# Optimization experiments

Hardware: AMD Instinct MI355X
Metric: run time of the kernel (lower is better)

Reference implementation:

```python
import jax, jax.numpy as jnp
import numpy as np

B, C, H, W = 16, 256, 56, 56
HEADS, DHEAD = 8, 32
INNER = HEADS * DHEAD  # == C
BLOCK, HALO = 7, 3
WIN = BLOCK + 2 * HALO      # 13
REL = WIN                   # rel_size = block + 2*halo
HIDDEN = 4 * C
EPS = 1e-6
LS_INIT = 1e-6


def layernorm2d(x, w, b):
    # channels-first LayerNorm over C, x: (B,C,H,W)
    u = jnp.mean(x, axis=1, keepdims=True)
    s = jnp.mean((x - u) ** 2, axis=1, keepdims=True)
    xn = (x - u) * jax.lax.rsqrt(s + EPS)
    return w[None, :, None, None] * xn + b[None, :, None, None]


def rel_to_abs(x):
    # x: (b, l, 2r-1) -> (b, l, r)
    b, l, m = x.shape
    r = (m + 1) // 2
    x = jnp.pad(x, ((0, 0), (0, 0), (0, 1))).reshape(b, l * (m + 1))
    x = jnp.pad(x, ((0, 0), (0, m - l))).reshape(b, l + 1, m)
    return x[:, :l, -r:]


def relative_logits_1d(q, rel_k):
    # q: (b, h, w, d); rel_k: (2r-1, d) -> (b, h, r, w, r)
    b, h, w, _ = q.shape
    r = (rel_k.shape[0] + 1) // 2
    logits = jnp.einsum('bxyd,rd->bxyr', q, rel_k)
    logits = rel_to_abs(logits.reshape(b * h, w, -1)).reshape(b, h, w, r)
    return jnp.broadcast_to(logits[:, :, None], (b, h, r, w, r))


def rel_pos_bias(q, rel_h, rel_w):
    b = q.shape[0]
    r = (rel_w.shape[0] + 1) // 2
    q2 = q.reshape(b, BLOCK, BLOCK, DHEAD)
    lw = relative_logits_1d(q2, rel_w)                        # (b, x, i, y, j)
    lw = lw.transpose(0, 1, 3, 2, 4).reshape(b, BLOCK * BLOCK, r * r)
    lh = relative_logits_1d(q2.transpose(0, 2, 1, 3), rel_h)  # (b, y, i, x, j)
    lh = lh.transpose(0, 3, 1, 4, 2).reshape(b, BLOCK * BLOCK, r * r)
    return lw + lh


def halo_attention(x, wq, wkv, wo, bo, rel_h, rel_w):
    Bq, _, Hh, Ww = x.shape
    nh, nw = Hh // BLOCK, Ww // BLOCK
    nb = nh * nw
    # queries: non-overlapping blocks -> (B*nb, BLOCK^2, C)
    q_inp = x.reshape(Bq, C, nh, BLOCK, nw, BLOCK).transpose(0, 2, 4, 3, 5, 1)
    q_inp = q_inp.reshape(Bq * nb, BLOCK * BLOCK, C)
    # keys/values: overlapping haloed windows (like F.unfold with padding=HALO)
    xp = jnp.pad(x, ((0, 0), (0, 0), (HALO, HALO), (HALO, HALO)))
    rows = (jnp.arange(nh) * BLOCK)[:, None] + jnp.arange(WIN)
    cols = (jnp.arange(nw) * BLOCK)[:, None] + jnp.arange(WIN)
    kv = xp[:, :, rows][:, :, :, :, cols]
    kv = kv.transpose(0, 2, 4, 3, 5, 1).reshape(Bq * nb, WIN * WIN, C)
    q = q_inp @ wq.T
    k, v = jnp.split(kv @ wkv.T, 2, axis=-1)

    def split_heads(t):
        b2, n2, _ = t.shape
        return t.reshape(b2, n2, HEADS, DHEAD).transpose(0, 2, 1, 3).reshape(b2 * HEADS, n2, DHEAD)

    q, k, v = map(split_heads, (q, k, v))
    q = q * (DHEAD ** -0.5)
    sim = jnp.einsum('bid,bjd->bij', q, k) + rel_pos_bias(q, rel_h, rel_w)
    # mask out-of-bounds (zero-padded) halo positions
    onep = jnp.pad(jnp.ones((Hh, Ww), sim.dtype), ((HALO, HALO), (HALO, HALO)))
    m = (onep[rows][:, :, cols].transpose(0, 2, 1, 3).reshape(nb, WIN * WIN)) > 0
    sim = sim.reshape(Bq, nb, HEADS, BLOCK * BLOCK, WIN * WIN)
    sim = jnp.where(m[None, :, None, None, :], sim, -jnp.finfo(sim.dtype).max)
    sim = sim.reshape(Bq * nb * HEADS, BLOCK * BLOCK, WIN * WIN)
    attn = jax.nn.softmax(sim, axis=-1)
    out = jnp.einsum('bij,bjd->bid', attn, v)
    out = out.reshape(Bq * nb, HEADS, BLOCK * BLOCK, DHEAD).transpose(0, 2, 1, 3)
    out = out.reshape(Bq * nb, BLOCK * BLOCK, INNER) @ wo.T + bo
    out = out.reshape(Bq, nh, nw, BLOCK, BLOCK, C).transpose(0, 5, 1, 3, 2, 4)
    return out.reshape(Bq, C, Hh, Ww)


def _forward(x, ln1_w, ln1_b, ln2_w, ln2_b, wq, wkv, wo, bo, rel_h, rel_w,
             gamma1, gamma2, fc1_w, fc1_b, fc2_w, fc2_b):
    y = halo_attention(layernorm2d(x, ln1_w, ln1_b), wq, wkv, wo, bo, rel_h, rel_w)
    x = x + gamma1 * y  # drop_path = 0 -> identity
    z = layernorm2d(x, ln2_w, ln2_b).transpose(0, 2, 3, 1)  # NHWC
    z = jax.nn.gelu(z @ fc1_w.T + fc1_b, approximate=False)
    z = z @ fc2_w.T + fc2_b
    z = gamma2 * z
    return x + z.transpose(0, 3, 1, 2)


def setup_inputs() -> dict:
    key = jax.random.key(0)
    ks = jax.random.split(key, 8)
    n = lambda k, sh: jax.random.normal(k, sh, jnp.float32) * 0.02
    scale = DHEAD ** -0.5
    return dict(
        x=jax.random.normal(ks[0], (B, C, H, W), jnp.float32),
        ln1_w=jnp.ones((C,), jnp.float32), ln1_b=jnp.zeros((C,), jnp.float32),
        ln2_w=jnp.ones((C,), jnp.float32), ln2_b=jnp.zeros((C,), jnp.float32),
        wq=n(ks[1], (INNER, C)),
        wkv=n(ks[2], (2 * INNER, C)),
        wo=n(ks[3], (C, INNER)), bo=jnp.zeros((C,), jnp.float32),
        rel_h=jax.random.normal(ks[4], (2 * REL - 1, DHEAD), jnp.float32) * scale,
        rel_w=jax.random.normal(ks[5], (2 * REL - 1, DHEAD), jnp.float32) * scale,
        gamma1=jnp.full((1, C, 1, 1), LS_INIT, jnp.float32),
        gamma2=jnp.full((1, 1, 1, C), LS_INIT, jnp.float32),
        fc1_w=n(ks[6], (HIDDEN, C)), fc1_b=jnp.zeros((HIDDEN,), jnp.float32),
        fc2_w=n(ks[7], (C, HIDDEN)), fc2_b=jnp.zeros((C,), jnp.float32),
    )


def reference(x, ln1_w, ln1_b, ln2_w, ln2_b, wq, wkv, wo, bo, rel_h, rel_w,
              gamma1, gamma2, fc1_w, fc1_b, fc2_w, fc2_b):
    return _forward(x, ln1_w, ln1_b, ln2_w, ln2_b, wq, wkv, wo, bo, rel_h, rel_w,
                    gamma1, gamma2, fc1_w, fc1_b, fc2_w, fc2_b)
```

## Files before the change

kernel.cpp:

```cpp
#include <hip/hip_runtime.h>
#include <cmath>

#define DI __device__ __forceinline__

typedef unsigned short ushort_t;
typedef __attribute__((ext_vector_type(8))) short short8;
typedef __attribute__((ext_vector_type(8))) unsigned short ushort8;
typedef __attribute__((ext_vector_type(4))) unsigned short ushort4_t;
typedef __attribute__((ext_vector_type(4))) float floatx4;
typedef unsigned int u32;
typedef __attribute__((ext_vector_type(4))) u32 uintx4;

DI float bf2f(ushort_t u) {
    unsigned v = ((unsigned)u) << 16;
    float f;
    __builtin_memcpy(&f, &v, 4);
    return f;
}
DI ushort_t f2bf(float f) {
    unsigned u;
    __builtin_memcpy(&u, &f, 4);
    unsigned r = (u + 0x7FFFu + ((u >> 16) & 1u)) >> 16;
    return (ushort_t)r;
}
DI ushort_t f2bf_tr(float f) {
    unsigned u;
    __builtin_memcpy(&u, &f, 4);
    return (ushort_t)(u >> 16);
}
DI u32 pack2bf(float lo, float hi) {
    u32 a, b;
    __builtin_memcpy(&a, &lo, 4);
    __builtin_memcpy(&b, &hi, 4);
    return (a >> 16) | (b & 0xFFFF0000u);
}

DI void async_copy16(const ushort_t* gsrc, ushort_t* ldst) {
    auto gp = (const __attribute__((address_space(1))) u32*)gsrc;
    auto lp = (__attribute__((address_space(3))) u32*)ldst;
    __builtin_amdgcn_global_load_lds(gp, lp, 16, 0, 0);
}


__global__ void convert_all_kernel(const float* __restrict__ wq, const float* __restrict__ wkv,
                                   const float* __restrict__ wo, const float* __restrict__ fc1w,
                                   const float* __restrict__ fc2w, const float* __restrict__ relh,
                                   const float* __restrict__ relw,
                                   ushort_t* __restrict__ bqkv, ushort_t* __restrict__ woC,
                                   ushort_t* __restrict__ fc1C, ushort_t* __restrict__ fc2C,
                                   ushort_t* __restrict__ relC, ushort_t* __restrict__ boneB) {
    int i = blockIdx.x * 256 + threadIdx.x;
    if (i < 196608) { bqkv[i] = f2bf(i < 65536 ? wq[i] : wkv[i - 65536]); return; }
    i -= 196608;
    if (i < 65536) { woC[i] = f2bf(wo[i]); return; }
    i -= 65536;
    if (i < 262144) { fc1C[i] = f2bf(fc1w[i]); return; }
    i -= 262144;
    if (i < 262144) { fc2C[i] = f2bf(fc2w[i]); return; }
    i -= 262144;
    if (i < 800) { relC[i] = f2bf(relh[i]); return; }
    i -= 800;
    if (i < 800) { relC[800 + i] = f2bf(relw[i]); return; }
    i -= 800;
    if (i < 5632) {
        int j = i >> 5, k = i & 31;
        int kh = j / 13, kw = j - kh * 13;
        ushort_t v = 0;
        if (j < 169) {
            if (k == kh || k == 13 + kw) v = 0x3F80;
            if (k == 28 && kh < 3) v = 0x3F80;
            if (k == 29 && kh >= 10) v = 0x3F80;
            if (k == 30 && kw < 3) v = 0x3F80;
            if (k == 31 && kw >= 10) v = 0x3F80;
        } else {
            if (k == 27) v = 0x3F80;
        }
        boneB[i] = v;
    }
}

__global__ __launch_bounds__(256) void ln1_kernel(const float* __restrict__ x,
                                                  const float* __restrict__ w,
                                                  const float* __restrict__ bias,
                                                  ushort_t* __restrict__ t1) {
    __shared__ __align__(16) float lds[56 * 256];
    int b = blockIdx.x / 56, h = blockIdx.x % 56;
    int c = threadIdx.x;
    const float* row = x + (((size_t)(b * 256 + c) * 56 + h) * 56);
    floatx4 vals[14];
#pragma unroll
    for (int i = 0; i < 14; i++) vals[i] = *(const floatx4*)(row + i * 4);
#pragma unroll
    for (int i = 0; i < 14; i++)
#pragma unroll
        for (int e = 0; e < 4; e++) lds[(i * 4 + e) * 256 + c] = vals[i][e];
    __syncthreads();
    int wv = threadIdx.x >> 6, lane = threadIdx.x & 63;
    for (int p0 = 0; p0 < 14; p0++) {
        int p = wv * 14 + p0;
        float xv[4];
        float s = 0.f, q = 0.f;
#pragma unroll
        for (int j = 0; j < 4; j++) {
            xv[j] = lds[p * 256 + lane * 4 + j];
            s += xv[j];
            q += xv[j] * xv[j];
        }
#pragma unroll
        for (int off = 32; off; off >>= 1) {
            s += __shfl_xor(s, off);
            q += __shfl_xor(q, off);
        }
        float mean = s * (1.f / 256.f);
        float var = q * (1.f / 256.f) - mean * mean;
        float rstd = rsqrtf(var + 1e-6f);
        size_t token = ((size_t)b * 56 + h) * 56 + p;
        ushort4_t o4;
#pragma unroll
        for (int j = 0; j < 4; j++) {
            int cc = lane * 4 + j;
            o4[j] = f2bf_tr(w[cc] * ((xv[j] - mean) * rstd) + bias[cc]);
        }
        *(ushort4_t*)(t1 + token * 256 + lane * 4) = o4;
    }
}

template <int EPI>
__global__ __launch_bounds__(256) void gemm_kernel(const ushort_t* __restrict__ A,
                                                   const ushort_t* __restrict__ Bw,
                                                   void* __restrict__ Cout, int K, int N,
                                                   const float* __restrict__ biasf,
                                                   const float* __restrict__ resf,
                                                   const float* __restrict__ gammaf,
                                                   int tok0) {
    __shared__ __align__(16) ushort_t As[2][128 * 32];
    __shared__ __align__(16) ushort_t Bs[2][128 * 32];
    int gy = gridDim.y;
    int lin = blockIdx.y * gridDim.x + blockIdx.x;
    int chunk = (gridDim.x * gy) >> 3;
    int wl = (lin & 7) * chunk + (lin >> 3);
    int mt = wl / gy;
    int m0 = mt * 128, n0 = (wl - mt * gy) * 128;
    int t = threadIdx.x;
    int wave = t >> 6, lane = t & 63;
    int wm = (wave & 1) * 64, wn = (wave >> 1) * 64;
    int lr = lane & 15, quad = lane >> 4;
    floatx4 acc[4][4] = {};

    int srow = t >> 2, sc16 = t & 3;
    int srow1 = srow + 64;
    const ushort_t* Arow0 = A + (size_t)(m0 + srow) * K + sc16 * 8;
    const ushort_t* Arow1 = A + (size_t)(m0 + srow1) * K + sc16 * 8;
    const ushort_t* Brow0 = Bw + (size_t)(n0 + srow) * K + sc16 * 8;
    const ushort_t* Brow1 = Bw + (size_t)(n0 + srow1) * K + sc16 * 8;

    async_copy16(Arow0, &As[0][t * 8]);
    async_copy16(Brow0, &Bs[0][t * 8]);
    async_copy16(Arow1, &As[0][(t + 256) * 8]);
    async_copy16(Brow1, &Bs[0][(t + 256) * 8]);
    __syncthreads();

    int cur = 0;
    for (int k0 = 0; k0 < K; k0 += 32) {
        if (k0 + 32 < K) {
            int nk = k0 + 32;
            async_copy16(Arow0 + nk, &As[cur ^ 1][t * 8]);
            async_copy16(Brow0 + nk, &Bs[cur ^ 1][t * 8]);
            async_copy16(Arow1 + nk, &As[cur ^ 1][(t + 256) * 8]);
            async_copy16(Brow1 + nk, &Bs[cur ^ 1][(t + 256) * 8]);
        }
        short8 af[4], bf[4];
#pragma unroll
        for (int i = 0; i < 4; i++) af[i] = *(const short8*)(&As[cur][(wm + i * 16 + lr) * 32 + quad * 8]);
#pragma unroll
        for (int i = 0; i < 4; i++) bf[i] = *(const short8*)(&Bs[cur][(wn + i * 16 + lr) * 32 + quad * 8]);
#pragma unroll
        for (int i = 0; i < 4; i++)
#pragma unroll
            for (int j = 0; j < 4; j++)
                acc[i][j] = __builtin_amdgcn_mfma_f32_16x16x32_bf16(af[i], bf[j], acc[i][j], 0, 0, 0);
        __syncthreads();
        cur ^= 1;
    }
    const float qsc = (EPI == 3 && n0 < 256) ? 0.17677669529663687f : 1.0f;
#pragma unroll
    for (int i = 0; i < 4; i++)
#pragma unroll
        for (int j = 0; j < 4; j++) {
            int row0 = m0 + wm + i * 16 + quad * 4;
            int col = n0 + wn + j * 16 + lr;
            if (EPI == 4) {
                int tokg = tok0 + row0;
                int bb = tokg / 3136;
                int rem = tokg - bb * 3136;
                floatx4 ov;
#pragma unroll
                for (int r = 0; r < 4; r++)
                    ov[r] = resf[(size_t)(row0 + r) * N + col] + gammaf[col] * (acc[i][j][r] + biasf[col]);
                *(floatx4*)((float*)Cout + (size_t)(bb * 256 + col) * 3136 + rem) = ov;
            } else if (EPI == 5) {
                int bb = row0 / 3136;
                int rem = row0 - bb * 3136;
                floatx4 rx = *(const floatx4*)(resf + (size_t)(bb * 256 + col) * 3136 + rem);
#pragma unroll
                for (int r = 0; r < 4; r++)
                    ((float*)Cout)[(size_t)(row0 + r) * N + col] =
                        rx[r] + gammaf[col] * (acc[i][j][r] + biasf[col]);
            } else if (EPI == 2) {
#pragma unroll
                for (int r = 0; r < 4; r++) {
                    float v = acc[i][j][r] + biasf[col];
                    float s = __expf(-1.702f * v);
                    v = v * __builtin_amdgcn_rcpf(1.0f + s);
                    ((ushort_t*)Cout)[(size_t)(row0 + r) * N + col] = f2bf_tr(v);
                }
            } else {
#pragma unroll
                for (int r = 0; r < 4; r++)
                    ((ushort_t*)Cout)[(size_t)(row0 + r) * N + col] = f2bf_tr(acc[i][j][r] * qsc);
            }
        }
}

__global__ __launch_bounds__(256, 4) void attn_kernel(const ushort_t* __restrict__ qkv,
                                                      const ushort_t* __restrict__ relh,
                                                      const ushort_t* __restrict__ relw,
                                                      const ushort_t* __restrict__ bone,
                                                      ushort_t* __restrict__ attnout) {
    __shared__ __align__(16) char smem[30208];
    ushort_t* Vt = (ushort_t*)smem;
    ushort_t* tblA = (ushort_t*)(smem + 12800);
    ushort_t* Ks = (ushort_t*)(smem + 16896);
    ushort_t* Ps = (ushort_t*)(smem + 16896);

    int wg = blockIdx.x;
    int head = wg & 7;
    int blk = (wg >> 3) & 63;
    int b = wg >> 9;
    int bh = blk >> 3, bw = blk & 7;
    int t = threadIdx.x;
    int wave = t >> 6, lane = t & 63;
    int lr = lane & 15, quad = lane >> 4;
    const int base_tok = b * 3136;

    short8 bbr[11];
#pragma unroll
    for (int nt = 0; nt < 11; nt++)
        bbr[nt] = *(const short8*)(bone + (nt * 16 + lr) * 32 + quad * 8);
    short8 bfg4[4];
#pragma unroll
    for (int ntile = 0; ntile < 4; ntile++) {
        int n = ntile * 16 + lr;
        int eff = (n < 50) ? n : 0;
        const ushort_t* rp = (eff < 25) ? (relh + eff * 32) : (relw + (eff - 25) * 32);
        bfg4[ntile] = *(const short8*)(rp + quad * 8);
    }
    short8 aq;
    {
        int qrow = wave * 16 + lr;
        int qx = qrow / 7, qy = qrow - qx * 7;
        int tok = min(base_tok + (bh * 7 + qx) * 56 + (bw * 7 + qy), 50175);
        aq = *(const short8*)(qkv + (size_t)tok * 768 + head * 32 + quad * 8);
    }

    ushort8 vv[3];
    int vrow[3], vcol[3];
#pragma unroll
    for (int it = 0; it < 3; it++) {
        int c = t + it * 256;
        bool act = (it < 2) || (t < 192);
        int j = c >> 2, ck = c & 3;
        int kh = j / 13, kw = j - kh * 13;
        int gh = bh * 7 + kh - 3, gw = bw * 7 + kw - 3;
        int tok = min(max(base_tok + gh * 56 + gw, 0), 50175);
        const ushort_t* src = qkv + (size_t)tok * 768 + head * 32 + ck * 8;
        if (act) {
            async_copy16(src + 256, Ks + c * 8);
            vv[it] = *(const ushort8*)(src + 512);
        }
        int nt = j >> 4, l2 = j & 15;
        int col = (nt >= 6) ? (96 + l2 * 6 + nt - 6) : (l2 * 6 + nt);
        vcol[it] = col ^ (ck << 3);
        vrow[it] = ck * 8;
    }
#pragma unroll
    for (int it = 0; it < 3; it++) {
        bool act = (it < 2) || (t < 192);
        if (act) {
#pragma unroll
            for (int e = 0; e < 8; e++) Vt[(vrow[it] + e) * 200 + vcol[it]] = vv[it][e];
        }
    }
#pragma unroll
    for (int i = 0; i < 2; i++) {
        int idx = t + i * 256;
        int row = idx >> 4, l2 = idx & 15;
        int col = 96 + l2 * 6 + 5;
        Vt[row * 200 + (col ^ ((row >> 3) << 3))] = 0;
    }
    {
        const u32 NEG = 0xCE6Eu;
        bool himask = (t & 3) == 3;
        u32 e1 = himask ? (NEG << 16) : 0u;
        u32 e2m = himask ? ((bh == 0 ? NEG : 0u) | (bh == 7 ? NEG << 16 : 0u)) : 0u;
        u32 e3m = himask ? ((bw == 0 ? NEG : 0u) | (bw == 7 ? NEG << 16 : 0u)) : 0u;
        uintx4 ini = {0u, e1, e2m, e3m};
        *(uintx4*)(smem + 12800 + t * 16) = ini;
    }
    __syncthreads();

    floatx4 zero4 = {0.f, 0.f, 0.f, 0.f};

    int qx_r[4], qy_r[4];
#pragma unroll
    for (int r = 0; r < 4; r++) {
        int row = wave * 16 + quad * 4 + r;
        qx_r[r] = row / 7;
        qy_r[r] = row - qx_r[r] * 7;
    }

#pragma unroll
    for (int ntile = 0; ntile < 4; ntile++) {
        int n = ntile * 16 + lr;
        floatx4 cta = __builtin_amdgcn_mfma_f32_16x16x32_bf16(aq, bfg4[ntile], zero4, 0, 0, 0);
#pragma unroll
        for (int r = 0; r < 4; r++) {
            int slot = (n < 25) ? (n - 12 + qx_r[r]) : (n - 24 + qy_r[r]);
            bool ok = (n < 25) ? (slot >= 0 && slot <= 12)
                               : (n < 50 && slot >= 13 && slot <= 25);
            int ss = ok ? slot : 26;
            tblA[(wave * 16 + quad * 4 + r) * 32 + ss] = f2bf_tr(cta[r]);
        }
    }

    short8 afb = *(const short8*)(tblA + (wave * 16 + lr) * 32 + quad * 8);
    floatx4 sacc[11];
#pragma unroll
    for (int nt = 0; nt < 11; nt++) {
        short8 bk = *(const short8*)(Ks + (nt * 16 + lr) * 32 + quad * 8);
        floatx4 s0 = __builtin_amdgcn_mfma_f32_16x16x32_bf16(aq, bk, zero4, 0, 0, 0);
        sacc[nt] = __builtin_amdgcn_mfma_f32_16x16x32_bf16(afb, bbr[nt], s0, 0, 0, 0);
    }

    __syncthreads();

    u32 phi[4][3];
#pragma unroll
    for (int r = 0; r < 4; r++) {
        int qr2 = wave * 16 + quad * 4 + r;
        float eb[11];
#pragma unroll
        for (int nt = 0; nt < 11; nt++) eb[nt] = __expf(sacc[nt][r]);
        u32* prow = (u32*)(Ps + qr2 * 104 + lr * 6);
        prow[0] = pack2bf(eb[0], eb[1]);
        prow[1] = pack2bf(eb[2], eb[3]);
        prow[2] = pack2bf(eb[4], eb[5]);
        phi[r][0] = pack2bf(eb[6], eb[7]);
        phi[r][1] = pack2bf(eb[8], eb[9]);
        phi[r][2] = pack2bf(eb[10], 0.f);
    }

    short8 ones8;
#pragma unroll
    for (int e = 0; e < 8; e++) ones8[e] = (short)0x3F80;

    floatx4 oacc[2] = {zero4, zero4};
    floatx4 osum = zero4;
#pragma unroll
    for (int kk = 0; kk < 3; kk++) {
        int k0 = kk * 32;
        short8 ap = *(const short8*)(Ps + (wave * 16 + lr) * 104 + k0 + quad * 8);
#pragma unroll
        for (int n2 = 0; n2 < 2; n2++) {
            int d = n2 * 16 + lr;
            int colb = (k0 + quad * 8) ^ ((d >> 3) << 3);
            short8 bv = *(const short8*)(Vt + d * 200 + colb);
            oacc[n2] = __builtin_amdgcn_mfma_f32_16x16x32_bf16(ap, bv, oacc[n2], 0, 0, 0);
        }
        osum = __builtin_amdgcn_mfma_f32_16x16x32_bf16(ap, ones8, osum, 0, 0, 0);
    }
#pragma unroll
    for (int r = 0; r < 4; r++) {
        int qr2 = wave * 16 + quad * 4 + r;
        u32* prow = (u32*)(Ps + qr2 * 104 + lr * 6);
        prow[0] = phi[r][0];
        prow[1] = phi[r][1];
        prow[2] = phi[r][2];
    }
#pragma unroll
    for (int kk = 0; kk < 3; kk++) {
        int k0 = kk * 32;
        short8 ap = *(const short8*)(Ps + (wave * 16 + lr) * 104 + k0 + quad * 8);
#pragma unroll
        for (int n2 = 0; n2 < 2; n2++) {
            int d = n2 * 16 + lr;
            int colb = (96 + k0 + quad * 8) ^ ((d >> 3) << 3);
            short8 bv = *(const short8*)(Vt + d * 200 + colb);
            oacc[n2] = __builtin_amdgcn_mfma_f32_16x16x32_bf16(ap, bv, oacc[n2], 0, 0, 0);
        }
        osum = __builtin_amdgcn_mfma_f32_16x16x32_bf16(ap, ones8, osum, 0, 0, 0);
    }

#pragma unroll
    for (int n2 = 0; n2 < 2; n2++)
#pragma unroll
        for (int r = 0; r < 4; r++) {
            int qr2 = wave * 16 + quad * 4 + r;
            if (qr2 < 49) {
                float inv = __builtin_amdgcn_rcpf(osum[r]);
                int qx = qr2 / 7, qy = qr2 - qx * 7;
                size_t tok = (size_t)base_tok + (bh * 7 + qx) * 56 + (bw * 7 + qy);
                attnout[tok * 256 + head * 32 + n2 * 16 + lr] = f2bf_tr(oacc[n2][r] * inv);
            }
        }
}

__global__ __launch_bounds__(256) void ln2_kernel(const float* __restrict__ xin,
                                                  const float* __restrict__ w,
                                                  const float* __restrict__ bias,
                                                  ushort_t* __restrict__ o) {
    int token = blockIdx.x * 4 + (threadIdx.x >> 6);
    int lane = threadIdx.x & 63;
    floatx4 v4 = *(const floatx4*)(xin + (size_t)token * 256 + lane * 4);
    float s = 0.f, q = 0.f;
#pragma unroll
    for (int i = 0; i < 4; i++) {
        s += v4[i];
        q += v4[i] * v4[i];
    }
#pragma unroll
    for (int off = 32; off; off >>= 1) {
        s += __shfl_xor(s, off);
        q += __shfl_xor(q, off);
    }
    float mean = s * (1.f / 256.f);
    float var = q * (1.f / 256.f) - mean * mean;
    float rstd = rsqrtf(var + 1e-6f);
    ushort4_t o4;
#pragma unroll
    for (int i = 0; i < 4; i++) {
        int c = lane * 4 + i;
        o4[i] = f2bf_tr(w[c] * ((v4[i] - mean) * rstd) + bias[c]);
    }
    *(ushort4_t*)(o + (size_t)token * 256 + lane * 4) = o4;
}

extern "C" void kernel_launch(void* const* d_in, const int* in_sizes, int n_in,
                              void* d_out, int out_size, void* d_ws, size_t ws_size,
                              hipStream_t stream) {
    const float* x = (const float*)d_in[0];
    const float* ln1w = (const float*)d_in[1];
    const float* ln1b = (const float*)d_in[2];
    const float* ln2w = (const float*)d_in[3];
    const float* ln2b = (const float*)d_in[4];
    const float* wq = (const float*)d_in[5];
    const float* wkv = (const float*)d_in[6];
    const float* wo = (const float*)d_in[7];
    const float* bo = (const float*)d_in[8];
    const float* relh = (const float*)d_in[9];
    const float* relw = (const float*)d_in[10];
    const float* g1 = (const float*)d_in[11];
    const float* g2 = (const float*)d_in[12];
    const float* fc1w = (const float*)d_in[13];
    const float* fc1b = (const float*)d_in[14];
    const float* fc2w = (const float*)d_in[15];
    const float* fc2b = (const float*)d_in[16];
    float* out = (float*)d_out;

    char* ws = (char*)d_ws;
    float* x1 = (float*)ws;
    ushort_t* t1 = (ushort_t*)(ws + 51380224);
    ushort_t* attnb = t1;
    ushort_t* qkv = (ushort_t*)(ws + 77070336);
    ushort_t* t2 = qkv;
    ushort_t* hid = (ushort_t*)(ws + 77070336 + 25690112);
    ushort_t* wv_ = (ushort_t*)(ws + 154140672);
    ushort_t* bqkv = wv_;
    ushort_t* woC = wv_ + 196608;
    ushort_t* fc1C = woC + 65536;
    ushort_t* fc2C = fc1C + 262144;
    ushort_t* relC = fc2C + 262144;
    ushort_t* boneG = relC + 1600;

    convert_all_kernel<<<3101, 256, 0, stream>>>(wq, wkv, wo, fc1w, fc2w, relh, relw,
                                                 bqkv, woC, fc1C, fc2C, relC, boneG);
    ln1_kernel<<<896, 256, 0, stream>>>(x, ln1w, ln1b, t1);
    gemm_kernel<3><<<dim3(392, 6), 256, 0, stream>>>(t1, bqkv, qkv, 256, 768, nullptr, nullptr, nullptr, 0);
    attn_kernel<<<8192, 256, 0, stream>>>(qkv, relC, relC + 800, boneG, attnb);
    gemm_kernel<5><<<dim3(392, 2), 256, 0, stream>>>(attnb, woC, x1, 256, 256, bo, x, g1, 0);
    ln2_kernel<<<12544, 256, 0, stream>>>(x1, ln2w, ln2b, t2);
    const size_t CH = 25088;
    for (int c = 0; c < 2; c++) {
        gemm_kernel<2><<<dim3(196, 8), 256, 0, stream>>>(t2 + c * CH * 256, fc1C, hid, 256, 1024, fc1b, nullptr, nullptr, 0);
        gemm_kernel<4><<<dim3(196, 2), 256, 0, stream>>>(hid, fc2C, out, 1024, 256, fc2b, x1 + c * CH * 256, g2, (int)(c * CH));
    }
}
```

Baseline: 386.5 us.

## Store MLP hidden activations and fc2 weights in FP8 and run fc2 with FP8 MFMA

Converts the fc2 weights to e4m3 FP8 and writes the fc1+GELU output as FP8 instead of bf16. The fc2 GEMM then uses the fp8 16x16x32 MFMA, which halves LDS and global traffic for its K=1024 operands. Because the hidden buffer is half the size, the two-chunk loop over tokens is merged into one launch each for fc1 and fc2. The trade-off is a large loss of precision on the hidden activations and fc2 weights, with no scaling applied, which risks failing the accuracy tolerance.

```diff
diff --git a/kernel.cpp b/kernel.cpp
--- a/kernel.cpp
+++ b/kernel.cpp
@@ -4,6 +4,7 @@
 #define DI __device__ __forceinline__
 
 typedef unsigned short ushort_t;
+typedef unsigned char u8;
 typedef __attribute__((ext_vector_type(8))) short short8;
 typedef __attribute__((ext_vector_type(8))) unsigned short ushort8;
 typedef __attribute__((ext_vector_type(4))) unsigned short ushort4_t;
@@ -34,8 +35,20 @@
     __builtin_memcpy(&b, &hi, 4);
     return (a >> 16) | (b & 0xFFFF0000u);
 }
-
-DI void async_copy16(const ushort_t* gsrc, ushort_t* ldst) {
+DI u8 f2e4m3(float f) {
+    u32 u;
+    __builtin_memcpy(&u, &f, 4);
+    u32 s = (u >> 24) & 0x80u;
+    u32 a = u & 0x7FFFFFFFu;
+    if (a < 0x3C800000u) return (u8)s;
+    if (a >= 0x43E00000u) return (u8)(s | 0x7E);
+    a += 0x7FFFFu + ((a >> 20) & 1u);
+    u32 e = (a >> 23) - 120u;
+    u32 m = (a >> 20) & 7u;
+    return (u8)(s | (e << 3) | m);
+}
+
+DI void async_copy16(const void* gsrc, void* ldst) {
     auto gp = (const __attribute__((address_space(1))) u32*)gsrc;
     auto lp = (__attribute__((address_space(3))) u32*)ldst;
     __builtin_amdgcn_global_load_lds(gp, lp, 16, 0, 0);
@@ -47,7 +60,7 @@
                                    const float* __restrict__ fc2w, const float* __restrict__ relh,
                                    const float* __restrict__ relw,
                                    ushort_t* __restrict__ bqkv, ushort_t* __restrict__ woC,
-                                   ushort_t* __restrict__ fc1C, ushort_t* __restrict__ fc2C,
+                                   ushort_t* __restrict__ fc1C, u8* __restrict__ fc2C8,
                                    ushort_t* __restrict__ relC, ushort_t* __restrict__ boneB) {
     int i = blockIdx.x * 256 + threadIdx.x;
     if (i < 196608) { bqkv[i] = f2bf(i < 65536 ? wq[i] : wkv[i - 65536]); return; }
@@ -56,7 +69,7 @@
     i -= 65536;
     if (i < 262144) { fc1C[i] = f2bf(fc1w[i]); return; }
     i -= 262144;
-    if (i < 262144) { fc2C[i] = f2bf(fc2w[i]); return; }
+    if (i < 262144) { fc2C8[i] = f2e4m3(fc2w[i]); return; }
     i -= 262144;
     if (i < 800) { relC[i] = f2bf(relh[i]); return; }
     i -= 800;
@@ -125,16 +138,17 @@
     }
 }
 
-template <int EPI>
-__global__ __launch_bounds__(256) void gemm_kernel(const ushort_t* __restrict__ A,
-                                                   const ushort_t* __restrict__ Bw,
+template <int EPI, int F8>
+__global__ __launch_bounds__(256) void gemm_kernel(const void* __restrict__ A,
+                                                   const void* __restrict__ Bw,
                                                    void* __restrict__ Cout, int K, int N,
                                                    const float* __restrict__ biasf,
                                                    const float* __restrict__ resf,
                                                    const float* __restrict__ gammaf,
                                                    int tok0) {
-    __shared__ __align__(16) ushort_t As[2][128 * 32];
-    __shared__ __align__(16) ushort_t Bs[2][128 * 32];
+    constexpr int ES = F8 ? 1 : 2;
+    __shared__ __align__(16) char As[2][128 * 32 * ES];
+    __shared__ __align__(16) char Bs[2][128 * 32 * ES];
     int gy = gridDim.y;
     int lin = blockIdx.y * gridDim.x + blockIdx.x;
     int chunk = (gridDim.x * gy) >> 3;
@@ -147,38 +161,62 @@
     int lr = lane & 15, quad = lane >> 4;
     floatx4 acc[4][4] = {};
 
-    int srow = t >> 2, sc16 = t & 3;
-    int srow1 = srow + 64;
-    const ushort_t* Arow0 = A + (size_t)(m0 + srow) * K + sc16 * 8;
-    const ushort_t* Arow1 = A + (size_t)(m0 + srow1) * K + sc16 * 8;
-    const ushort_t* Brow0 = Bw + (size_t)(n0 + srow) * K + sc16 * 8;
-    const ushort_t* Brow1 = Bw + (size_t)(n0 + srow1) * K + sc16 * 8;
-
-    async_copy16(Arow0, &As[0][t * 8]);
-    async_copy16(Brow0, &Bs[0][t * 8]);
-    async_copy16(Arow1, &As[0][(t + 256) * 8]);
-    async_copy16(Brow1, &Bs[0][(t + 256) * 8]);
+    const char* A8 = (const char*)A;
+    const char* B8 = (const char*)Bw;
+    const size_t rbA = (size_t)K * ES;
+
+    int cpr = 2 * ES;
+    int r0 = t / cpr, o0 = (t % cpr) * 16;
+    int r1 = (t + 256) / cpr, o1 = ((t + 256) % cpr) * 16;
+    const char* Ar0 = A8 + (size_t)(m0 + r0) * rbA + o0;
+    const char* Br0 = B8 + (size_t)(n0 + r0) * rbA + o0;
+    const char* Ar1 = A8 + (size_t)(m0 + r1) * rbA + o1;
+    const char* Br1 = B8 + (size_t)(n0 + r1) * rbA + o1;
+
+    async_copy16(Ar0, &As[0][t * 16]);
+    async_copy16(Br0, &Bs[0][t * 16]);
+    if constexpr (!F8) {
+        async_copy16(Ar1, &As[0][(t + 256) * 16]);
+        async_copy16(Br1, &Bs[0][(t + 256) * 16]);
+    }
     __syncthreads();
 
     int cur = 0;
     for (int k0 = 0; k0 < K; k0 += 32) {
         if (k0 + 32 < K) {
-            int nk = k0 + 32;
-            async_copy16(Arow0 + nk, &As[cur ^ 1][t * 8]);
-            async_copy16(Brow0 + nk, &Bs[cur ^ 1][t * 8]);
-            async_copy16(Arow1 + nk, &As[cur ^ 1][(t + 256) * 8]);
-            async_copy16(Brow1 + nk, &Bs[cur ^ 1][(t + 256) * 8]);
-        }
-        short8 af[4], bf[4];
-#pragma unroll
-        for (int i = 0; i < 4; i++) af[i] = *(const short8*)(&As[cur][(wm + i * 16 + lr) * 32 + quad * 8]);
-#pragma unroll
-        for (int i = 0; i < 4; i++) bf[i] = *(const short8*)(&Bs[cur][(wn + i * 16 + lr) * 32 + quad * 8]);
-#pragma unroll
-        for (int i = 0; i < 4; i++)
-#pragma unroll
-            for (int j = 0; j < 4; j++)
-                acc[i][j] = __builtin_amdgcn_mfma_f32_16x16x32_bf16(af[i], bf[j], acc[i][j], 0, 0, 0);
+            size_t nb = (size_t)32 * ES;
+            async_copy16(Ar0 + (k0 / 32 + 1) * nb, &As[cur ^ 1][t * 16]);
+            async_copy16(Br0 + (k0 / 32 + 1) * nb, &Bs[cur ^ 1][t * 16]);
+            if constexpr (!F8) {
+                async_copy16(Ar1 + (k0 / 32 + 1) * nb, &As[cur ^ 1][(t + 256) * 16]);
+                async_copy16(Br1 + (k0 / 32 + 1) * nb, &Bs[cur ^ 1][(t + 256) * 16]);
+            }
+        }
+        if constexpr (F8) {
+            long af[4], bf[4];
+#pragma unroll
+            for (int i = 0; i < 4; i++)
+                __builtin_memcpy(&af[i], &As[cur][(wm + i * 16 + lr) * 32 + quad * 8], 8);
+#pragma unroll
+            for (int i = 0; i < 4; i++)
+                __builtin_memcpy(&bf[i], &Bs[cur][(wn + i * 16 + lr) * 32 + quad * 8], 8);
+#pragma unroll
+            for (int i = 0; i < 4; i++)
+#pragma unroll
+                for (int j = 0; j < 4; j++)
+                    acc[i][j] = __builtin_amdgcn_mfma_f32_16x16x32_fp8_fp8(af[i], bf[j], acc[i][j], 0, 0, 0);
+        } else {
+            short8 af[4], bf[4];
+#pragma unroll
+            for (int i = 0; i < 4; i++) af[i] = *(const short8*)(&As[cur][(wm + i * 16 + lr) * 64 + quad * 16]);
+#pragma unroll
+            for (int i = 0; i < 4; i++) bf[i] = *(const short8*)(&Bs[cur][(wn + i * 16 + lr) * 64 + quad * 16]);
+#pragma unroll
+            for (int i = 0; i < 4; i++)
+#pragma unroll
+                for (int j = 0; j < 4; j++)
+                    acc[i][j] = __builtin_amdgcn_mfma_f32_16x16x32_bf16(af[i], bf[j], acc[i][j], 0, 0, 0);
+        }
         __syncthreads();
         cur ^= 1;
     }
@@ -206,13 +244,13 @@
                 for (int r = 0; r < 4; r++)
                     ((float*)Cout)[(size_t)(row0 + r) * N + col] =
                         rx[r] + gammaf[col] * (acc[i][j][r] + biasf[col]);
-            } else if (EPI == 2) {
+            } else if (EPI == 6) {
 #pragma unroll
                 for (int r = 0; r < 4; r++) {
                     float v = acc[i][j][r] + biasf[col];
                     float s = __expf(-1.702f * v);
                     v = v * __builtin_amdgcn_rcpf(1.0f + s);
-                    ((ushort_t*)Cout)[(size_t)(row0 + r) * N + col] = f2bf_tr(v);
+                    ((u8*)Cout)[(size_t)(row0 + r) * N + col] = f2e4m3(v);
                 }
             } else {
 #pragma unroll
@@ -473,7 +511,7 @@
     ushort_t* attnb = t1;
     ushort_t* qkv = (ushort_t*)(ws + 77070336);
     ushort_t* t2 = qkv;
-    ushort_t* hid = (ushort_t*)(ws + 77070336 + 25690112);
+    u8* hid8 = (u8*)(ws + 102760448);
     ushort_t* wv_ = (ushort_t*)(ws + 154140672);
     ushort_t* bqkv = wv_;
     ushort_t* woC = wv_ + 196608;
@@ -483,15 +521,12 @@
     ushort_t* boneG = relC + 1600;
 
     convert_all_kernel<<<3101, 256, 0, stream>>>(wq, wkv, wo, fc1w, fc2w, relh, relw,
-                                                 bqkv, woC, fc1C, fc2C, relC, boneG);
+                                                 bqkv, woC, fc1C, (u8*)fc2C, relC, boneG);
     ln1_kernel<<<896, 256, 0, stream>>>(x, ln1w, ln1b, t1);
-    gemm_kernel<3><<<dim3(392, 6), 256, 0, stream>>>(t1, bqkv, qkv, 256, 768, nullptr, nullptr, nullptr, 0);
+    gemm_kernel<3, 0><<<dim3(392, 6), 256, 0, stream>>>(t1, bqkv, qkv, 256, 768, nullptr, nullptr, nullptr, 0);
     attn_kernel<<<8192, 256, 0, stream>>>(qkv, relC, relC + 800, boneG, attnb);
-    gemm_kernel<5><<<dim3(392, 2), 256, 0, stream>>>(attnb, woC, x1, 256, 256, bo, x, g1, 0);
+    gemm_kernel<5, 0><<<dim3(392, 2), 256, 0, stream>>>(attnb, woC, x1, 256, 256, bo, x, g1, 0);
     ln2_kernel<<<12544, 256, 0, stream>>>(x1, ln2w, ln2b, t2);
-    const size_t CH = 25088;
-    for (int c = 0; c < 2; c++) {
-        gemm_kernel<2><<<dim3(196, 8), 256, 0, stream>>>(t2 + c * CH * 256, fc1C, hid, 256, 1024, fc1b, nullptr, nullptr, 0);
-        gemm_kernel<4><<<dim3(196, 2), 256, 0, stream>>>(hid, fc2C, out, 1024, 256, fc2b, x1 + c * CH * 256, g2, (int)(c * CH));
-    }
-}
+    gemm_kernel<6, 0><<<dim3(392, 8), 256, 0, stream>>>(t2, fc1C, hid8, 256, 1024, fc1b, nullptr, nullptr, 0);
+    gemm_kernel<4, 1><<<dim3(392, 2), 256, 0, stream>>>(hid8, (u8*)fc2C, out, 1024, 256, fc2b, x1, g2, 0);
+}
```

Result: no change. 386.2 us (-0.1%).
